# Kernel tuning notes

Hardware: AMD Instinct MI355X
Metric: run time of the kernel (lower is better)

Reference implementation:

```python
import jax, jax.numpy as jnp
from jax import lax
import numpy as np

B, S, FD, FS, H = 256, 365, 32, 27, 256


def setup_inputs() -> dict:
    key = jax.random.key(0)
    ks = jax.random.split(key, 6)
    x_d = jax.random.normal(ks[0], (B, S, FD), dtype=jnp.float32)
    x_s = jax.random.normal(ks[1], (B, FS), dtype=jnp.float32)
    W_ih = jax.random.normal(ks[2], (FD, 3 * H), dtype=jnp.float32) * 0.1
    W_hh = jnp.tile(jnp.eye(H, dtype=jnp.float32), (1, 3)) + 0.01 * jax.random.normal(ks[3], (H, 3 * H), dtype=jnp.float32)
    W_sh = jax.random.normal(ks[4], (FS, H), dtype=jnp.float32) * 0.1
    bias = jnp.zeros((3 * H,), dtype=jnp.float32).at[:H].set(5.0)  # initial_forget_bias=5
    bias_s = jnp.zeros((H,), dtype=jnp.float32)
    W_fc = jax.random.normal(ks[5], (H, 1), dtype=jnp.float32) * 0.1
    b_fc = jnp.zeros((1,), dtype=jnp.float32)
    return {"x_d": x_d, "x_s": x_s, "W_ih": W_ih, "W_hh": W_hh, "W_sh": W_sh,
            "bias": bias, "bias_s": bias_s, "W_fc": W_fc, "b_fc": b_fc}


def _ealstm(x_d, x_s, W_ih, W_hh, W_sh, bias, bias_s):
    # static input gate, computed once: [B, H]
    i_gate = jax.nn.sigmoid(x_s @ W_sh + bias_s)
    # precompute dynamic input projection, time-major: [S, B, 3H]
    x_proj = jnp.einsum('bsd,dh->sbh', x_d, W_ih)
    Hh = W_hh.shape[0]
    Bb = x_d.shape[0]

    def step(carry, xt):
        h, c = carry
        gates = h @ W_hh + bias + xt  # [B, 3H]
        f, o, g = jnp.split(gates, 3, axis=1)
        c1 = jax.nn.sigmoid(f) * c + i_gate * jnp.tanh(g)
        h1 = jax.nn.sigmoid(o) * jnp.tanh(c1)
        return (h1, c1), (h1, c1)

    init = (jnp.zeros((Bb, Hh), x_d.dtype), jnp.zeros((Bb, Hh), x_d.dtype))
    _, (h_n, c_n) = lax.scan(step, init, x_proj)
    # time-major -> batch-first
    return jnp.transpose(h_n, (1, 0, 2)), jnp.transpose(c_n, (1, 0, 2))


def reference(x_d, x_s, W_ih, W_hh, W_sh, bias, bias_s, W_fc, b_fc):
    h_n, c_n = _ealstm(x_d, x_s, W_ih, W_hh, W_sh, bias, bias_s)
    # dropout p=0.0 -> identity; fc head: [B, S, 1]
    out = h_n @ W_fc + b_fc
    return (out, h_n, c_n)
```

## Files before the change

kernel.cpp:

```cpp
#include <hip/hip_runtime.h>


#define BB 256
#define SS 365
#define FD 32
#define FS 27
#define HH 256
#define G3 768
#define KTOT 288
#define KQ 4
#define KCH 72
#define NA 192
#define PPITCH 776

__global__ __launch_bounds__(768) void ealstm_kernel(
    const float* __restrict__ x_d, const float* __restrict__ x_s,
    const float* __restrict__ W_ih, const float* __restrict__ W_hh,
    const float* __restrict__ W_sh, const float* __restrict__ bias,
    const float* __restrict__ bias_s, const float* __restrict__ W_fc,
    const float* __restrict__ b_fc, float* __restrict__ d_out)
{
    __shared__ __align__(16) float hbuf[KTOT];
    __shared__ __align__(16) float partials[KQ][PPITCH];
    __shared__ float outp[4];

    const int t = threadIdx.x;
    const int b = blockIdx.x;
    const int kq = t / NA;
    const int a  = t - kq * NA;
    const int col4 = 4 * a;

    float4 w[KCH];
#pragma unroll
    for (int i = 0; i < KCH; ++i) {
        const int k = kq * KCH + i;
        const float* src = (k < HH) ? (W_hh + (size_t)k * G3 + col4)
                                    : (W_ih + (size_t)(k - HH) * G3 + col4);
        w[i] = *reinterpret_cast<const float4*>(src);
    }

    float c_state = 0.f, ig = 0.f, bf = 0.f, bo = 0.f, bg = 0.f, wfc = 0.f;
    if (t < HH) {
        float accs = bias_s[t];
        for (int k = 0; k < FS; ++k)
            accs = fmaf(x_s[(size_t)b * FS + k], W_sh[(size_t)k * HH + t], accs);
        ig = 1.f / (1.f + __expf(-accs));
        bf = bias[t]; bo = bias[t + HH]; bg = bias[t + 2 * HH];
        wfc = W_fc[t];
        hbuf[t] = 0.f;
    }
    if (t >= 512 && t < 512 + FD) {
        hbuf[HH + (t - 512)] = x_d[(size_t)b * SS * FD + (t - 512)];
    }
    const float bfc = b_fc[0];
    __syncthreads();

    float* __restrict__ out_fc = d_out;
    float* __restrict__ hn_out = d_out + (size_t)BB * SS;
    float* __restrict__ cn_out = hn_out + (size_t)BB * SS * HH;

    for (int s = 0; s < SS; ++s) {
        float4 acc = make_float4(0.f, 0.f, 0.f, 0.f);
        const float4* hv4 = reinterpret_cast<const float4*>(hbuf + kq * KCH);
#pragma unroll
        for (int i = 0; i < KCH / 4; ++i) {
            const float4 hv = hv4[i];
            acc.x = fmaf(hv.x, w[4 * i + 0].x, acc.x);
            acc.y = fmaf(hv.x, w[4 * i + 0].y, acc.y);
            acc.z = fmaf(hv.x, w[4 * i + 0].z, acc.z);
            acc.w = fmaf(hv.x, w[4 * i + 0].w, acc.w);
            acc.x = fmaf(hv.y, w[4 * i + 1].x, acc.x);
            acc.y = fmaf(hv.y, w[4 * i + 1].y, acc.y);
            acc.z = fmaf(hv.y, w[4 * i + 1].z, acc.z);
            acc.w = fmaf(hv.y, w[4 * i + 1].w, acc.w);
            acc.x = fmaf(hv.z, w[4 * i + 2].x, acc.x);
            acc.y = fmaf(hv.z, w[4 * i + 2].y, acc.y);
            acc.z = fmaf(hv.z, w[4 * i + 2].z, acc.z);
            acc.w = fmaf(hv.z, w[4 * i + 2].w, acc.w);
            acc.x = fmaf(hv.w, w[4 * i + 3].x, acc.x);
            acc.y = fmaf(hv.w, w[4 * i + 3].y, acc.y);
            acc.z = fmaf(hv.w, w[4 * i + 3].z, acc.z);
            acc.w = fmaf(hv.w, w[4 * i + 3].w, acc.w);
        }
        *reinterpret_cast<float4*>(&partials[kq][col4]) = acc;
        __syncthreads();

        if (t < HH) {
            float f = partials[0][t] + partials[1][t] + partials[2][t] + partials[3][t] + bf;
            float o = partials[0][t + HH] + partials[1][t + HH] + partials[2][t + HH] + partials[3][t + HH] + bo;
            float g = partials[0][t + 2 * HH] + partials[1][t + 2 * HH] + partials[2][t + 2 * HH] + partials[3][t + 2 * HH] + bg;
            const float sf = 1.f / (1.f + __expf(-f));
            const float so = 1.f / (1.f + __expf(-o));
            const float tg = 1.f - 2.f / (1.f + __expf(2.f * g));
            c_state = sf * c_state + ig * tg;
            const float tc = 1.f - 2.f / (1.f + __expf(2.f * c_state));
            const float h1 = so * tc;
            hbuf[t] = h1;
            const size_t oidx = ((size_t)b * SS + s) * HH + t;
            hn_out[oidx] = h1;
            cn_out[oidx] = c_state;
            float p = h1 * wfc;
            for (int d = 32; d > 0; d >>= 1) p += __shfl_down(p, d);
            if ((t & 63) == 0) outp[t >> 6] = p;
        } else if (t >= 512 && t < 512 + FD) {
            const int sn = (s + 1 < SS) ? (s + 1) : s;
            hbuf[HH + (t - 512)] = x_d[(size_t)b * SS * FD + (size_t)sn * FD + (t - 512)];
        }
        __syncthreads();
        if (t == 0) {
            out_fc[(size_t)b * SS + s] = outp[0] + outp[1] + outp[2] + outp[3] + bfc;
        }
    }
}

extern "C" void kernel_launch(void* const* d_in, const int* in_sizes, int n_in,
                              void* d_out, int out_size, void* d_ws, size_t ws_size,
                              hipStream_t stream) {
    const float* x_d    = (const float*)d_in[0];
    const float* x_s    = (const float*)d_in[1];
    const float* W_ih   = (const float*)d_in[2];
    const float* W_hh   = (const float*)d_in[3];
    const float* W_sh   = (const float*)d_in[4];
    const float* bias   = (const float*)d_in[5];
    const float* bias_s = (const float*)d_in[6];
    const float* W_fc   = (const float*)d_in[7];
    const float* b_fc   = (const float*)d_in[8];

    ealstm_kernel<<<dim3(BB), dim3(768), 0, stream>>>(
        x_d, x_s, W_ih, W_hh, W_sh, bias, bias_s, W_fc, b_fc, (float*)d_out);
}
```

Baseline: 6.281 ms.

## Split recurrent weights across registers, LDS and streamed global loads with 512 threads

Cuts the block from 768 to 512 threads. Each thread now owns one hidden unit's three gates over half the K dimension (144 rows) and holds those weights in three tiers: 68 rows in registers, 24 rows in LDS, and the rest reloaded from global/L2 every step with double-buffered prefetch. The partial-sum reduction drops from 4 to 2 partials, and per-thread constants move to shared memory to free registers. The aim is to keep weight storage within the register budget while reducing the reduction and sync cost. In exchange it adds repeated global weight traffic on every timestep of the serial recurrence.

```diff
diff --git a/kernel.cpp b/kernel.cpp
--- a/kernel.cpp
+++ b/kernel.cpp
@@ -7,50 +7,89 @@
 #define FS 27
 #define HH 256
 #define G3 768
-#define KTOT 288
-#define KQ 4
-#define KCH 72
-#define NA 192
-#define PPITCH 776
+#define KCH 144
+#define RV 68
+#define RL 24
+#define NQS 13
 
-__global__ __launch_bounds__(768) void ealstm_kernel(
+#define FMA12(v, h4) do { \
+    acc0 = fmaf((v)[0],  (h4).x, acc0); acc1 = fmaf((v)[1],  (h4).x, acc1); acc2 = fmaf((v)[2],  (h4).x, acc2); \
+    acc0 = fmaf((v)[3],  (h4).y, acc0); acc1 = fmaf((v)[4],  (h4).y, acc1); acc2 = fmaf((v)[5],  (h4).y, acc2); \
+    acc0 = fmaf((v)[6],  (h4).z, acc0); acc1 = fmaf((v)[7],  (h4).z, acc1); acc2 = fmaf((v)[8],  (h4).z, acc2); \
+    acc0 = fmaf((v)[9],  (h4).w, acc0); acc1 = fmaf((v)[10], (h4).w, acc1); acc2 = fmaf((v)[11], (h4).w, acc2); \
+} while (0)
+
+#define LOADQ(buf, kst) do { \
+    _Pragma("unroll") \
+    for (int rr_ = 0; rr_ < 4; ++rr_) { \
+        const int k_ = (kst) + rr_; \
+        const float* p_ = (k_ < HH) ? (W_hh + (size_t)k_ * G3) \
+                                    : (W_ih + (size_t)(k_ - HH) * G3); \
+        (buf)[3*rr_+0] = p_[a]; \
+        (buf)[3*rr_+1] = p_[a + 256]; \
+        (buf)[3*rr_+2] = p_[a + 512]; \
+    } \
+} while (0)
+
+__device__ __forceinline__ float sigmoidf_(float x) {
+    return 1.f / (1.f + __expf(-x));
+}
+__device__ __forceinline__ float tanhf_(float x) {
+    return 1.f - 2.f / (1.f + __expf(2.f * x));
+}
+
+__global__ __launch_bounds__(512) void ealstm_kernel(
     const float* __restrict__ x_d, const float* __restrict__ x_s,
     const float* __restrict__ W_ih, const float* __restrict__ W_hh,
     const float* __restrict__ W_sh, const float* __restrict__ bias,
     const float* __restrict__ bias_s, const float* __restrict__ W_fc,
     const float* __restrict__ b_fc, float* __restrict__ d_out)
 {
-    __shared__ __align__(16) float hbuf[KTOT];
-    __shared__ __align__(16) float partials[KQ][PPITCH];
+    __shared__ float4 lds_w[18][512];
+    __shared__ __align__(16) float hbuf[HH + FD];
+    __shared__ float partials[2][3][HH];
+    __shared__ float gatec[5][HH];
     __shared__ float outp[4];
 
     const int t = threadIdx.x;
     const int b = blockIdx.x;
-    const int kq = t / NA;
-    const int a  = t - kq * NA;
-    const int col4 = 4 * a;
+    const int kq = t >> 8;
+    const int a  = t & 255;
+    const int kbase = kq * KCH;
+    const int sbase = kbase + RV + RL;
 
-    float4 w[KCH];
+    float wv[RV * 3];
 #pragma unroll
-    for (int i = 0; i < KCH; ++i) {
-        const int k = kq * KCH + i;
-        const float* src = (k < HH) ? (W_hh + (size_t)k * G3 + col4)
-                                    : (W_ih + (size_t)(k - HH) * G3 + col4);
-        w[i] = *reinterpret_cast<const float4*>(src);
+    for (int r = 0; r < RV; ++r) {
+        const float* p = W_hh + (size_t)(kbase + r) * G3;
+        wv[3*r+0] = p[a];
+        wv[3*r+1] = p[a + 256];
+        wv[3*r+2] = p[a + 512];
     }
 
-    float c_state = 0.f, ig = 0.f, bf = 0.f, bo = 0.f, bg = 0.f, wfc = 0.f;
+#pragma unroll
+    for (int j = 0; j < 18; ++j) {
+        float tmp[4];
+#pragma unroll
+        for (int e = 0; e < 4; ++e) {
+            const int i = 4*j + e, r = i / 3, g = i - 3*r;
+            tmp[e] = W_hh[(size_t)(kbase + RV + r) * G3 + g*256 + a];
+        }
+        lds_w[j][t] = make_float4(tmp[0], tmp[1], tmp[2], tmp[3]);
+    }
+
     if (t < HH) {
         float accs = bias_s[t];
         for (int k = 0; k < FS; ++k)
             accs = fmaf(x_s[(size_t)b * FS + k], W_sh[(size_t)k * HH + t], accs);
-        ig = 1.f / (1.f + __expf(-accs));
-        bf = bias[t]; bo = bias[t + HH]; bg = bias[t + 2 * HH];
-        wfc = W_fc[t];
+        gatec[0][t] = sigmoidf_(accs);
+        gatec[1][t] = bias[t];
+        gatec[2][t] = bias[t + HH];
+        gatec[3][t] = bias[t + 2*HH];
+        gatec[4][t] = W_fc[t];
         hbuf[t] = 0.f;
-    }
-    if (t >= 512 && t < 512 + FD) {
-        hbuf[HH + (t - 512)] = x_d[(size_t)b * SS * FD + (t - 512)];
+    } else if (t < HH + FD) {
+        hbuf[t] = x_d[(size_t)b * SS * FD + (t - HH)];
     }
     const float bfc = b_fc[0];
     __syncthreads();
@@ -59,52 +98,68 @@
     float* __restrict__ hn_out = d_out + (size_t)BB * SS;
     float* __restrict__ cn_out = hn_out + (size_t)BB * SS * HH;
 
+    float c_state = 0.f;
+    const float4* hq = reinterpret_cast<const float4*>(hbuf);
+
     for (int s = 0; s < SS; ++s) {
-        float4 acc = make_float4(0.f, 0.f, 0.f, 0.f);
-        const float4* hv4 = reinterpret_cast<const float4*>(hbuf + kq * KCH);
+        float acc0 = 0.f, acc1 = 0.f, acc2 = 0.f;
+
+        float va[12], vb[12];
+        LOADQ(va, sbase + 0);
+        LOADQ(vb, sbase + 4);
+
 #pragma unroll
-        for (int i = 0; i < KCH / 4; ++i) {
-            const float4 hv = hv4[i];
-            acc.x = fmaf(hv.x, w[4 * i + 0].x, acc.x);
-            acc.y = fmaf(hv.x, w[4 * i + 0].y, acc.y);
-            acc.z = fmaf(hv.x, w[4 * i + 0].z, acc.z);
-            acc.w = fmaf(hv.x, w[4 * i + 0].w, acc.w);
-            acc.x = fmaf(hv.y, w[4 * i + 1].x, acc.x);
-            acc.y = fmaf(hv.y, w[4 * i + 1].y, acc.y);
-            acc.z = fmaf(hv.y, w[4 * i + 1].z, acc.z);
-            acc.w = fmaf(hv.y, w[4 * i + 1].w, acc.w);
-            acc.x = fmaf(hv.z, w[4 * i + 2].x, acc.x);
-            acc.y = fmaf(hv.z, w[4 * i + 2].y, acc.y);
-            acc.z = fmaf(hv.z, w[4 * i + 2].z, acc.z);
-            acc.w = fmaf(hv.z, w[4 * i + 2].w, acc.w);
-            acc.x = fmaf(hv.w, w[4 * i + 3].x, acc.x);
-            acc.y = fmaf(hv.w, w[4 * i + 3].y, acc.y);
-            acc.z = fmaf(hv.w, w[4 * i + 3].z, acc.z);
-            acc.w = fmaf(hv.w, w[4 * i + 3].w, acc.w);
+        for (int q = 0; q < 17; ++q) {
+            const float4 h4 = hq[kbase/4 + q];
+            FMA12(&wv[12*q], h4);
         }
-        *reinterpret_cast<float4*>(&partials[kq][col4]) = acc;
+#pragma unroll
+        for (int m = 0; m < 6; ++m) {
+            const float4 q0 = lds_w[3*m+0][t];
+            const float4 q1 = lds_w[3*m+1][t];
+            const float4 q2 = lds_w[3*m+2][t];
+            const float v[12] = {q0.x,q0.y,q0.z,q0.w, q1.x,q1.y,q1.z,q1.w,
+                                 q2.x,q2.y,q2.z,q2.w};
+            const float4 h4 = hq[(kbase + RV)/4 + m];
+            FMA12(v, h4);
+        }
+#pragma unroll
+        for (int m = 0; m < NQS; ++m) {
+            const float4 h4 = hq[sbase/4 + m];
+            if (m & 1) {
+                FMA12(vb, h4);
+                if (m + 2 < NQS) LOADQ(vb, sbase + 4*(m + 2));
+            } else {
+                FMA12(va, h4);
+                if (m + 2 < NQS) LOADQ(va, sbase + 4*(m + 2));
+            }
+        }
+
+        partials[kq][0][a] = acc0;
+        partials[kq][1][a] = acc1;
+        partials[kq][2][a] = acc2;
         __syncthreads();
 
         if (t < HH) {
-            float f = partials[0][t] + partials[1][t] + partials[2][t] + partials[3][t] + bf;
-            float o = partials[0][t + HH] + partials[1][t + HH] + partials[2][t + HH] + partials[3][t + HH] + bo;
-            float g = partials[0][t + 2 * HH] + partials[1][t + 2 * HH] + partials[2][t + 2 * HH] + partials[3][t + 2 * HH] + bg;
-            const float sf = 1.f / (1.f + __expf(-f));
-            const float so = 1.f / (1.f + __expf(-o));
-            const float tg = 1.f - 2.f / (1.f + __expf(2.f * g));
-            c_state = sf * c_state + ig * tg;
-            const float tc = 1.f - 2.f / (1.f + __expf(2.f * c_state));
+            const float f = partials[0][0][t] + partials[1][0][t] + gatec[1][t];
+            const float o = partials[0][1][t] + partials[1][1][t] + gatec[2][t];
+            const float g = partials[0][2][t] + partials[1][2][t] + gatec[3][t];
+            const float sf = sigmoidf_(f);
+            const float so = sigmoidf_(o);
+            const float tg = tanhf_(g);
+            c_state = sf * c_state + gatec[0][t] * tg;
+            const float tc = tanhf_(c_state);
             const float h1 = so * tc;
             hbuf[t] = h1;
             const size_t oidx = ((size_t)b * SS + s) * HH + t;
             hn_out[oidx] = h1;
             cn_out[oidx] = c_state;
-            float p = h1 * wfc;
+            float p = h1 * gatec[4][t];
             for (int d = 32; d > 0; d >>= 1) p += __shfl_down(p, d);
             if ((t & 63) == 0) outp[t >> 6] = p;
-        } else if (t >= 512 && t < 512 + FD) {
+        } else if (t < HH + FD) {
             const int sn = (s + 1 < SS) ? (s + 1) : s;
-            hbuf[HH + (t - 512)] = x_d[(size_t)b * SS * FD + (size_t)sn * FD + (t - 512)];
+            hbuf[t] = x_d[(size_t)b * SS * FD + (size_t)sn * FD + (t - HH)];
         }
         __syncthreads();
         if (t == 0) {
@@ -126,6 +181,6 @@
     const float* W_fc   = (const float*)d_in[7];
     const float* b_fc   = (const float*)d_in[8];
 
-    ealstm_kernel<<<dim3(BB), dim3(768), 0, stream>>>(
+    ealstm_kernel<<<dim3(BB), dim3(512), 0, stream>>>(
         x_d, x_s, W_ih, W_hh, W_sh, bias, bias_s, W_fc, b_fc, (float*)d_out);
 }
```

New measurement: 14.91 ms. +137.4%, slower.
